# Optimization experiments

Hardware: AMD Instinct MI355X
Metric: run time of the kernel (lower is better)

Reference implementation:

```python
import jax, jax.numpy as jnp
import numpy as np

NL, B, L, D, H, KH, FF, M, NCT, ND = 8, 4, 512, 512, 16, 32, 2048, 512, 6, 14
BINS = jnp.arange(10.0, 150.0, 10.0)  # 14 bucket boundaries
SCALE = 1.0 / np.sqrt(KH).astype(np.float32)


def setup_inputs() -> dict:
    key = jax.random.key(0)
    ks = iter(jax.random.split(key, 64))
    nrm = lambda shape, s=0.02: jax.random.normal(next(ks), shape, dtype=jnp.float32) * s
    inp = {}
    inp['cell_types'] = jax.random.randint(next(ks), (B, L), 0, NCT)
    inp['distances'] = jax.random.uniform(next(ks), (B, L, L), dtype=jnp.float32) * 139.0
    inp['cell_emb'] = nrm((NCT, D), 1.0)
    for name in ['Kqk', 'Kqr', 'Kkr', 'Vqk', 'Vqr', 'Vkr']:
        inp[name] = nrm((ND, KH), 0.02)
    for name in ['Wq', 'Wk', 'Wv', 'Wo']:
        inp[name] = nrm((NL, D, D))
    for name in ['bq', 'bk', 'bv', 'bo']:
        inp[name] = jnp.zeros((NL, D), dtype=jnp.float32)
    inp['W1'] = nrm((NL, D, FF)); inp['b1'] = jnp.zeros((NL, FF), dtype=jnp.float32)
    inp['W2'] = nrm((NL, FF, D)); inp['b2'] = jnp.zeros((NL, D), dtype=jnp.float32)
    inp['g1'] = jnp.ones((NL, D), dtype=jnp.float32); inp['be1'] = jnp.zeros((NL, D), dtype=jnp.float32)
    inp['g2'] = jnp.ones((NL, D), dtype=jnp.float32); inp['be2'] = jnp.zeros((NL, D), dtype=jnp.float32)
    inp['Wm1'] = nrm((D, M)); inp['bm1'] = jnp.zeros((M,), dtype=jnp.float32)
    inp['Wm2'] = nrm((M, 1)); inp['bm2'] = jnp.zeros((1,), dtype=jnp.float32)
    return inp


def _layernorm(x, g, b, eps=1e-5):
    mu = x.mean(-1, keepdims=True)
    var = ((x - mu) ** 2).mean(-1, keepdims=True)
    return (x - mu) * jax.lax.rsqrt(var + eps) * g + b


def _forward(cell_types, distances, cell_emb, Kqk, Kqr, Kkr, Vqk, Vqr, Vkr,
             Wq, bq, Wk, bk, Wv, bv, Wo, bo, W1, b1, W2, b2, g1, be1, g2, be2,
             Wm1, bm1, Wm2, bm2):
    Bsz, Ls = cell_types.shape
    # torch.bucketize(right=False) == searchsorted side='left'
    didx = jnp.clip(jnp.searchsorted(BINS, distances, side='left'), 0, ND - 1)  # [B,L,L]
    # gather distance-bucket relative embeddings once; shared across all layers
    Eqk = Kqk[didx]                      # [B,L,L,KH]  query-side score bias
    Eqr = Kqr[didx]                      # [B,L,L,KH]  key-side score bias
    Ekr = Kkr[didx].sum(-1)              # [B,L,L]     pure pairwise score bias
    Vbias = Vqk[didx] + Vqr[didx] + Vkr[didx]  # [B,L,L,KH] additive value bias
    h = cell_emb[cell_types]             # [B,L,D]

    def layer(h, p):
        wq, bq_, wk, bk_, wv, bv_, wo, bo_, w1, b1_, w2, b2_, gg1, bb1, gg2, bb2 = p
        q = (h @ wq + bq_).reshape(Bsz, Ls, H, KH)
        k = (h @ wk + bk_).reshape(Bsz, Ls, H, KH)
        v = (h @ wv + bv_).reshape(Bsz, Ls, H, KH)
        e = jnp.einsum('blhk,bxhk->bhlx', q, k)
        e = e + jnp.einsum('blhk,blxk->bhlx', q, Eqk)
        e = e + jnp.einsum('bxhk,blxk->bhlx', k, Eqr)
        e = e + Ekr[:, None, :, :]
        a = jax.nn.softmax(e * SCALE, axis=-1)  # [B,H,L,L]
        z = jnp.einsum('bhlx,bxhk->blhk', a, v) + jnp.einsum('bhlx,blxk->blhk', a, Vbias)
        o = z.reshape(Bsz, Ls, H * KH) @ wo + bo_
        h2 = _layernorm(h + o, gg1, bb1)  # post-norm (norm_first=False)
        f = jax.nn.gelu(h2 @ w1 + b1_, approximate=False) @ w2 + b2_
        return _layernorm(h2 + f, gg2, bb2), None

    h, _ = jax.lax.scan(layer, h, (Wq, bq, Wk, bk, Wv, bv, Wo, bo,
                                   W1, b1, W2, b2, g1, be1, g2, be2))
    pooled = h.sum(axis=1)                      # [B,D]
    return jax.nn.relu(pooled @ Wm1 + bm1) @ Wm2 + bm2  # [B,1]


def reference(cell_types, distances, cell_emb, Kqk, Kqr, Kkr, Vqk, Vqr, Vkr,
              Wq, bq, Wk, bk, Wv, bv, Wo, bo, W1, b1, W2, b2, g1, be1, g2, be2,
              Wm1, bm1, Wm2, bm2):
    return _forward(cell_types, distances, cell_emb, Kqk, Kqr, Kkr, Vqk, Vqr, Vkr,
                    Wq, bq, Wk, bk, Wv, bv, Wo, bo, W1, b1, W2, b2, g1, be1, g2, be2,
                    Wm1, bm1, Wm2, bm2)
```

## Files before the change

### kernel.cpp

```cpp
#include <hip/hip_runtime.h>
#include <math.h>

#define NLAY 8
#define BB 4
#define LL 512
#define DDIM 512
#define HH 16
#define KHD 32
#define FFD 2048
#define MMD 512
#define NDB 14
#define QKS 1536
#define SCALEF 0.17677669529663687f

typedef unsigned short u16;
typedef unsigned int u32;
typedef __attribute__((ext_vector_type(8))) short bf16x8;
typedef __attribute__((ext_vector_type(4))) float f32x4;
typedef __attribute__((ext_vector_type(4))) u32 u32x4;

__device__ __forceinline__ u16 f2bf(float f) {
  unsigned u = __builtin_bit_cast(unsigned, f);
  u = (u + 0x7fffu + ((u >> 16) & 1u)) >> 16;
  return (u16)u;
}
__device__ __forceinline__ float bf2f(u16 v) {
  unsigned u = ((unsigned)v) << 16;
  return __builtin_bit_cast(float, u);
}
__device__ __forceinline__ u32 cvt_pk_bf16(float lo, float hi) {
  u32 r;
  asm("v_cvt_pk_bf16_f32 %0, %1, %2" : "=v"(r) : "v"(lo), "v"(hi));
  return r;
}
__device__ __forceinline__ float wredSum(float v) {
#pragma unroll
  for (int o = 32; o > 0; o >>= 1) v += __shfl_down(v, o);
  return v;
}
__device__ __forceinline__ void gload_lds16(const u16* g, u16* l) {
  __builtin_amdgcn_global_load_lds((const __attribute__((address_space(1))) void*)g,
                                   (__attribute__((address_space(3))) void*)l, 16, 0, 0);
}

__global__ void bucketize_kernel(const float* __restrict__ dist, unsigned char* __restrict__ didx, int n) {
  int i = blockIdx.x * 256 + threadIdx.x;
  if (i >= n) return;
  float4 v = ((const float4*)dist)[i];
  float vv[4] = {v.x, v.y, v.z, v.w};
  unsigned char o[4];
#pragma unroll
  for (int j = 0; j < 4; ++j) {
    int c = 0;
#pragma unroll
    for (int s = 1; s <= NDB; ++s) c += (10.0f * (float)s < vv[j]) ? 1 : 0;
    o[j] = (unsigned char)(c > (NDB - 1) ? (NDB - 1) : c);
  }
  *(uchar4*)(didx + i * 4) = *(uchar4*)o;
}

__global__ void embed_kernel(const int* __restrict__ ct, const float* __restrict__ emb,
                             float* __restrict__ h, u16* __restrict__ hbf, int n) {
  int i = blockIdx.x * 256 + threadIdx.x;
  if (i >= n) return;
  int bl = i >> 9, d = i & 511;
  float v = emb[ct[bl] * DDIM + d];
  h[i] = v;
  hbf[i] = f2bf(v);
}

__global__ void prep_kernel(const float* __restrict__ Vqk, const float* __restrict__ Vqr,
                            const float* __restrict__ Vkr, const float* __restrict__ Kkr,
                            float* __restrict__ Vsum, float* __restrict__ EkrS) {
  int tid = threadIdx.x;
  if (tid < NDB * KHD) Vsum[tid] = Vqk[tid] + Vqr[tid] + Vkr[tid];
  if (tid < NDB) {
    float s = 0.f;
    for (int kk = 0; kk < KHD; ++kk) s += Kkr[tid * KHD + kk];
    EkrS[tid] = s;
  }
}

__global__ void biaspack_kernel(const float* __restrict__ bq, const float* __restrict__ bk,
                                const float* __restrict__ bv, float* __restrict__ bqkv) {
  int i = blockIdx.x * 256 + threadIdx.x;
  if (i >= NLAY * QKS) return;
  int lay = i / QKS, c = i % QKS;
  float v;
  if (c < 512) v = bq[lay * DDIM + c];
  else if (c < 1024) v = bk[lay * DDIM + c - 512];
  else v = bv[lay * DDIM + c - 1024];
  bqkv[i] = v;
}

__device__ __forceinline__ void wtconv_tile(const float* __restrict__ src, u16* __restrict__ dst,
                                            int K, int N, int tn, int tk) {
  __shared__ float tl[64][65];
  const int t = threadIdx.x;
#pragma unroll
  for (int p = 0; p < 4; ++p) {
    int k = tk * 64 + p * 16 + (t >> 4);
    int n = tn * 64 + (t & 15) * 4;
    float4 v = *(const float4*)(src + (size_t)k * N + n);
    tl[(t & 15) * 4 + 0][p * 16 + (t >> 4)] = v.x;
    tl[(t & 15) * 4 + 1][p * 16 + (t >> 4)] = v.y;
    tl[(t & 15) * 4 + 2][p * 16 + (t >> 4)] = v.z;
    tl[(t & 15) * 4 + 3][p * 16 + (t >> 4)] = v.w;
  }
  __syncthreads();
  int n = t >> 2, cc = t & 3;
  u16 o[16];
#pragma unroll
  for (int e = 0; e < 16; ++e) o[e] = f2bf(tl[n][cc * 16 + e]);
  u16* dp = dst + (size_t)(tn * 64 + n) * K + tk * 64 + cc * 16;
  *(uint4*)(dp) = *(uint4*)&o[0];
  *(uint4*)(dp + 8) = *(uint4*)&o[8];
}

__global__ __launch_bounds__(256) void wconv_layer(
    const float* __restrict__ Wq, const float* __restrict__ Wk, const float* __restrict__ Wv,
    const float* __restrict__ Wo, const float* __restrict__ W1, const float* __restrict__ W2,
    u16* __restrict__ Wqkvt, u16* __restrict__ Wot, u16* __restrict__ W1t, u16* __restrict__ W2t) {
  int b = blockIdx.x;
  if (b < 64) { wtconv_tile(Wq, Wqkvt, 512, 512, b >> 3, b & 7); return; }
  if (b < 128) { b -= 64; wtconv_tile(Wk, Wqkvt + 512 * 512, 512, 512, b >> 3, b & 7); return; }
  if (b < 192) { b -= 128; wtconv_tile(Wv, Wqkvt + 1024 * 512, 512, 512, b >> 3, b & 7); return; }
  if (b < 256) { b -= 192; wtconv_tile(Wo, Wot, 512, 512, b >> 3, b & 7); return; }
  if (b < 512) { b -= 256; wtconv_tile(W1, W1t, 512, FFD, b >> 3, b & 7); return; }
  b -= 512; wtconv_tile(W2, W2t, FFD, 512, b >> 5, b & 31);
}

__global__ __launch_bounds__(256) void gemm_bf16(
    const u16* __restrict__ A, const u16* __restrict__ Bt, const float* __restrict__ bias,
    float* __restrict__ Cf, u16* __restrict__ Cb,
    int M, int N, int K, int act, int scaleLT) {
  __shared__ u16 As[32 * 64];
  __shared__ u16 Bs[64 * 64];
  const int tid = threadIdx.x, w = tid >> 6, lane = tid & 63;
  const int lr = lane & 15, lg = lane >> 4;
  const int wr = w >> 1, wc = w & 1;
  const int gx = N >> 6;
  const int bi = blockIdx.x;
  const int xcd = bi & 7, rr = bi >> 3;
  const int y = xcd * 8 + rr / gx, x = rr % gx;
  const int row0 = y * 32, col0 = x * 64;
  const int srow = lane >> 3;
  const int aoff = ((lane & 7) ^ srow) * 8;
  const f32x4 z4 = {0.f, 0.f, 0.f, 0.f};
  f32x4 acc[2] = {z4, z4};

  for (int k0 = 0; k0 < K; k0 += 64) {
    gload_lds16(A + (size_t)(row0 + w * 8 + srow) * K + k0 + aoff, As + (w * 8) * 64);
#pragma unroll
    for (int i = 0; i < 2; ++i)
      gload_lds16(Bt + (size_t)(col0 + w * 16 + i * 8 + srow) * K + k0 + aoff,
                  Bs + (w * 16 + i * 8) * 64);
    __syncthreads();
#pragma unroll
    for (int kh = 0; kh < 2; ++kh) {
      bf16x8 a, b[2];
      {
        int r = wr * 16 + lr;
        a = *(const bf16x8*)(As + r * 64 + (((kh * 4 + lg) ^ (r & 7)) << 3));
      }
#pragma unroll
      for (int ni = 0; ni < 2; ++ni) {
        int r = wc * 32 + ni * 16 + lr;
        b[ni] = *(const bf16x8*)(Bs + r * 64 + (((kh * 4 + lg) ^ (r & 7)) << 3));
      }
#pragma unroll
      for (int ni = 0; ni < 2; ++ni)
        acc[ni] = __builtin_amdgcn_mfma_f32_16x16x32_bf16(a, b[ni], acc[ni], 0, 0, 0);
    }
    __syncthreads();
  }
  {
    int r = row0 + wr * 16 + lg * 4;
#pragma unroll
    for (int ni = 0; ni < 2; ++ni) {
      int c = col0 + wc * 32 + ni * 16 + lr;
      float bs = bias[c];
      float sc = (c < scaleLT) ? SCALEF : 1.0f;
#pragma unroll
      for (int j = 0; j < 4; ++j) {
        float v = acc[ni][j] + bs;
        if (act == 1) v = 0.5f * v * (1.0f + erff(v * 0.70710678118654752f));
        size_t idx = (size_t)(r + j) * N + c;
        if (Cf) Cf[idx] = v;
        if (Cb) Cb[idx] = f2bf(v * sc);
      }
    }
  }
}

__global__ void proj_qk_kernel(const u16* __restrict__ qkv, const float* __restrict__ Kqk,
                               const float* __restrict__ Kqr, const float* __restrict__ ekrs,
                               float* __restrict__ qE2, u16* __restrict__ kEbf) {
  int idx = blockIdx.x * 256 + threadIdx.x;
  if (idx >= BB * HH * LL * NDB) return;
  int d = idx % NDB;
  int rest = idx / NDB;
  int l = rest & (LL - 1);
  int bh = rest >> 9;
  int h = bh & (HH - 1);
  int b = bh >> 4;
  const u16* qr_ = qkv + ((size_t)(b * LL + l)) * QKS + h * KHD;
  const u16* kr_ = qr_ + 512;
  const float* kq = Kqk + d * KHD;
  const float* kk2 = Kqr + d * KHD;
  float sq = 0.f, sk = 0.f;
#pragma unroll
  for (int kk = 0; kk < KHD; ++kk) {
    sq += bf2f(qr_[kk]) * kq[kk];
    sk += bf2f(kr_[kk]) * kk2[kk];
  }
  qE2[idx] = sq;
  kEbf[(size_t)rest * 16 + d] = f2bf(sk * SCALEF + SCALEF * ekrs[d]);
}

__global__ __launch_bounds__(256) void vtrans_kernel(const u16* __restrict__ qkv, u16* __restrict__ vt) {
  const int h = blockIdx.x, b = blockIdx.y, tid = threadIdx.x;
  __shared__ u16 tile[KHD][520];
  for (int it = 0; it < 64; ++it) {
    int idx = it * 256 + tid;
    int x = idx >> 5, kh = idx & 31;
    tile[kh][x] = qkv[((size_t)(b * LL) + x) * QKS + 1024 + h * KHD + kh];
  }
  __syncthreads();
  int r = tid >> 3, seg = tid & 7;
  uint4* dst = (uint4*)(vt + ((size_t)(b * HH + h) * KHD + r) * LL);
  const uint4* src = (const uint4*)(&tile[r][0]);
#pragma unroll
  for (int j = 0; j < 8; ++j) dst[seg + j * 8] = src[seg + j * 8];
}

__global__ __launch_bounds__(256) void attn_exp_kernel(
    const u16* __restrict__ qkv, const float* __restrict__ qE2, const u16* __restrict__ kEbf,
    const unsigned char* __restrict__ didx, const float* __restrict__ Vsum,
    u16* __restrict__ E, float* __restrict__ vbias, float* __restrict__ invs) {
  const int i = blockIdx.x;
  const int j = i >> 3;
  const int g = (i & 7) * 8 + (j >> 5);
  const int qr = j & 31;
  const int h = g & 15, b = g >> 4;
  const int tid = threadIdx.x, lane = tid & 63, w = tid >> 6;
  const int lr = lane & 15, lg = lane >> 4;
  const int row0 = qr * 16;

  __shared__ u16 kEs[LL][18];
  __shared__ float qEs[16][17];
  __shared__ float hist[4][64][17];

  {
    const u32* gs = (const u32*)(kEbf + (((size_t)(b * HH + h)) * LL) * 16);
    u32* ls = (u32*)(&kEs[0][0]);
#pragma unroll
    for (int t = 0; t < 16; ++t) {
      int idx = t * 256 + tid;
      int r = idx >> 3, c = idx & 7;
      ls[r * 9 + c] = gs[idx];
    }
  }
  if (tid < 224) {
    int r = tid / 14, d = tid % 14;
    qEs[r][d] = qE2[(((size_t)(b * HH + h)) * LL + row0 + r) * NDB + d];
  }
  {
    float* hf = &hist[0][0][0];
#pragma unroll
    for (int t = 0; t < 17; ++t) hf[t * 256 + tid] = 0.f;
  }

  const bf16x8 aQ = *(const bf16x8*)(qkv + ((size_t)(b * LL + row0 + lr)) * QKS + h * KHD + lg * 8);

  __syncthreads();

  const f32x4 zero4 = {0.f, 0.f, 0.f, 0.f};
  const int keyA = 8 * (lr >> 2) + (lr & 3);
  const u16* kbase = qkv + (size_t)b * LL * QKS + 512 + h * KHD + lg * 8;
  const unsigned char* drow = didx + ((size_t)(b * LL) + row0 + lr) * LL + 8 * lg;
  u16* Ebase = E + ((((size_t)(b * HH + h)) * LL) + row0 + lr) * LL + 8 * lg;
  float* hlane = &hist[w][lane][0];

  bf16x8 kA[4], kB[4];
  uint2 dv[4];
#pragma unroll
  for (int ct = 0; ct < 4; ++ct) {
    const int x0 = w * 128 + ct * 32;
    kA[ct] = *(const bf16x8*)(kbase + (size_t)(x0 + keyA) * QKS);
    kB[ct] = *(const bf16x8*)(kbase + (size_t)(x0 + keyA + 4) * QKS);
    dv[ct] = *(const uint2*)(drow + x0);
  }
  __builtin_amdgcn_sched_barrier(0);

#pragma unroll
  for (int ct = 0; ct < 4; ++ct) {
    const int x0 = w * 128 + ct * 32;
    f32x4 sA = __builtin_amdgcn_mfma_f32_16x16x32_bf16(kA[ct], aQ, zero4, 0, 0, 0);
    f32x4 sB = __builtin_amdgcn_mfma_f32_16x16x32_bf16(kB[ct], aQ, zero4, 0, 0, 0);
    float pA[4], pB[4];
#pragma unroll
    for (int q = 0; q < 4; ++q) {
      const int da = (dv[ct].x >> (8 * q)) & 0xff;
      const int db = (dv[ct].y >> (8 * q)) & 0xff;
      pA[q] = __expf(sA[q] + qEs[lr][da] + bf2f(kEs[x0 + 8 * lg + q][da]));
      pB[q] = __expf(sB[q] + qEs[lr][db] + bf2f(kEs[x0 + 8 * lg + 4 + q][db]));
      hlane[da] += pA[q];
      hlane[db] += pB[q];
    }
    u32x4 pw;
    pw[0] = cvt_pk_bf16(pA[0], pA[1]);
    pw[1] = cvt_pk_bf16(pA[2], pA[3]);
    pw[2] = cvt_pk_bf16(pB[0], pB[1]);
    pw[3] = cvt_pk_bf16(pB[2], pB[3]);
    *(u32x4*)(Ebase + x0) = pw;
  }

  __syncthreads();

  const int r = tid >> 4, c = tid & 15;
  float ht[NDB];
  float rsum = 0.f;
#pragma unroll
  for (int d = 0; d < NDB; ++d) {
    float a = 0.f;
#pragma unroll
    for (int ww = 0; ww < 4; ++ww)
#pragma unroll
      for (int gg = 0; gg < 4; ++gg) a += hist[ww][r + 16 * gg][d];
    ht[d] = a;
    rsum += a;
  }
  float vb_0 = 0.f, vb_1 = 0.f;
#pragma unroll
  for (int d = 0; d < NDB; ++d) {
    vb_0 += ht[d] * Vsum[d * KHD + c];
    vb_1 += ht[d] * Vsum[d * KHD + 16 + c];
  }
  const size_t rowi = (((size_t)(b * HH + h)) * LL) + row0 + r;
  vbias[rowi * KHD + c] = vb_0;
  vbias[rowi * KHD + 16 + c] = vb_1;
  if (c == 0) invs[rowi] = 1.0f / rsum;
}

__global__ __launch_bounds__(256) void attn_pv_kernel(
    const u16* __restrict__ E, const u16* __restrict__ vtbf,
    const float* __restrict__ vbias, const float* __restrict__ invs,
    u16* __restrict__ z) {
  const int i = blockIdx.x;
  const int j = i >> 3;
  const int g = (i & 7) * 8 + (j >> 3);
  const int qt = j & 7;
  const int h = g & 15, b = g >> 4;
  const int tid = threadIdx.x, lane = tid & 63, w = tid >> 6;
  const int lr = lane & 15, lg = lane >> 4;
  const int row0 = qt * 64 + w * 16;

  f32x4 o0 = {0.f, 0.f, 0.f, 0.f}, o1 = {0.f, 0.f, 0.f, 0.f};
  const u16* Ebase = E + ((((size_t)(b * HH + h)) * LL) + row0 + lr) * LL + lg * 8;
  const u16* vbase = vtbf + ((size_t)(b * HH + h) * KHD) * LL + lg * 8;

#pragma unroll 4
  for (int ct = 0; ct < 16; ++ct) {
    const int x0 = ct * 32;
    bf16x8 aE = *(const bf16x8*)(Ebase + x0);
    bf16x8 vb0 = *(const bf16x8*)(vbase + (size_t)lr * LL + x0);
    bf16x8 vb1 = *(const bf16x8*)(vbase + (size_t)(16 + lr) * LL + x0);
    o0 = __builtin_amdgcn_mfma_f32_16x16x32_bf16(aE, vb0, o0, 0, 0, 0);
    o1 = __builtin_amdgcn_mfma_f32_16x16x32_bf16(aE, vb1, o1, 0, 0, 0);
  }

#pragma unroll
  for (int q = 0; q < 4; ++q) {
    const int rl = lg * 4 + q;
    const size_t rowi = (((size_t)(b * HH + h)) * LL) + row0 + rl;
    const float inv = invs[rowi];
    const float v0 = vbias[rowi * KHD + lr];
    const float v1 = vbias[rowi * KHD + 16 + lr];
    const size_t orow = ((size_t)(b * LL + row0 + rl)) * DDIM + h * KHD;
    z[orow + lr] = f2bf((o0[q] + v0) * inv);
    z[orow + 16 + lr] = f2bf((o1[q] + v1) * inv);
  }
}

__global__ __launch_bounds__(256) void add_ln_kernel(
    const float* __restrict__ X, const float* __restrict__ Y,
    const float* __restrict__ g, const float* __restrict__ be,
    float* __restrict__ out, u16* __restrict__ outb) {
  const int row = blockIdx.x, tid = threadIdx.x;
  const int lane = tid & 63, wid = tid >> 6;
  __shared__ float red[4];
  const size_t base = (size_t)row * DDIM;
  float x0 = X[base + tid] + Y[base + tid];
  float x1 = X[base + tid + 256] + Y[base + tid + 256];
  float s = wredSum(x0 + x1);
  if (lane == 0) red[wid] = s;
  __syncthreads();
  float mu = (red[0] + red[1] + red[2] + red[3]) * (1.0f / DDIM);
  __syncthreads();
  float d0 = x0 - mu, d1 = x1 - mu;
  float vs = wredSum(d0 * d0 + d1 * d1);
  if (lane == 0) red[wid] = vs;
  __syncthreads();
  float var = (red[0] + red[1] + red[2] + red[3]) * (1.0f / DDIM);
  float inv = rsqrtf(var + 1e-5f);
  float r0 = d0 * inv * g[tid] + be[tid];
  float r1 = d1 * inv * g[tid + 256] + be[tid + 256];
  out[base + tid] = r0;
  out[base + tid + 256] = r1;
  outb[base + tid] = f2bf(r0);
  outb[base + tid + 256] = f2bf(r1);
}

__global__ __launch_bounds__(256) void pool2_kernel(const float* __restrict__ h, float* __restrict__ pooled) {
  const int s = blockIdx.x, b = blockIdx.y, tid = threadIdx.x;
  float a0 = 0.f, a1 = 0.f;
  const float* base = h + ((size_t)(b * LL) + s * 64) * DDIM;
#pragma unroll 4
  for (int l = 0; l < 64; ++l) {
    a0 += base[(size_t)l * DDIM + tid];
    a1 += base[(size_t)l * DDIM + tid + 256];
  }
  atomicAdd(&pooled[b * DDIM + tid], a0);
  atomicAdd(&pooled[b * DDIM + tid + 256], a1);
}

__global__ __launch_bounds__(256) void head1_kernel(
    const float* __restrict__ pooled, const float* __restrict__ Wm1, float* __restrict__ hidden) {
  const int s = blockIdx.x, b = blockIdx.y, tid = threadIdx.x;
  __shared__ float pl[64];
  if (tid < 64) pl[tid] = pooled[b * DDIM + s * 64 + tid];
  __syncthreads();
  float a0 = 0.f, a1 = 0.f;
  const float* wbase = Wm1 + (size_t)(s * 64) * MMD;
#pragma unroll 8
  for (int dd = 0; dd < 64; ++dd) {
    float p = pl[dd];
    a0 += p * wbase[(size_t)dd * MMD + tid];
    a1 += p * wbase[(size_t)dd * MMD + tid + 256];
  }
  atomicAdd(&hidden[b * MMD + tid], a0);
  atomicAdd(&hidden[b * MMD + tid + 256], a1);
}

__global__ __launch_bounds__(256) void head2_kernel(
    const float* __restrict__ hidden, const float* __restrict__ bm1,
    const float* __restrict__ Wm2, const float* __restrict__ bm2, float* __restrict__ out) {
  const int b = blockIdx.x, tid = threadIdx.x;
  float part = 0.f;
#pragma unroll
  for (int jj = 0; jj < 2; ++jj) {
    int j = tid + jj * 256;
    part += fmaxf(hidden[b * MMD + j] + bm1[j], 0.f) * Wm2[j];
  }
  __shared__ float red[4];
  int lane = tid & 63, wid = tid >> 6;
  float ssum = wredSum(part);
  if (lane == 0) red[wid] = ssum;
  __syncthreads();
  if (tid == 0) out[b] = red[0] + red[1] + red[2] + red[3] + bm2[0];
}

extern "C" void kernel_launch(void* const* d_in, const int* in_sizes, int n_in,
                              void* d_out, int out_size, void* d_ws, size_t ws_size,
                              hipStream_t stream) {
  const int* cell_types = (const int*)d_in[0];
  const float* distances = (const float*)d_in[1];
  const float* cell_emb = (const float*)d_in[2];
  const float* Kqk = (const float*)d_in[3];
  const float* Kqr = (const float*)d_in[4];
  const float* Kkr = (const float*)d_in[5];
  const float* Vqk = (const float*)d_in[6];
  const float* Vqr = (const float*)d_in[7];
  const float* Vkr = (const float*)d_in[8];
  const float* Wq = (const float*)d_in[9];
  const float* Wk = (const float*)d_in[10];
  const float* Wv = (const float*)d_in[11];
  const float* Wo = (const float*)d_in[12];
  const float* bq = (const float*)d_in[13];
  const float* bk = (const float*)d_in[14];
  const float* bv = (const float*)d_in[15];
  const float* bo = (const float*)d_in[16];
  const float* W1 = (const float*)d_in[17];
  const float* b1 = (const float*)d_in[18];
  const float* W2 = (const float*)d_in[19];
  const float* b2 = (const float*)d_in[20];
  const float* g1 = (const float*)d_in[21];
  const float* be1 = (const float*)d_in[22];
  const float* g2 = (const float*)d_in[23];
  const float* be2 = (const float*)d_in[24];
  const float* Wm1 = (const float*)d_in[25];
  const float* bm1 = (const float*)d_in[26];
  const float* Wm2 = (const float*)d_in[27];
  const float* bm2 = (const float*)d_in[28];

  char* w = (char*)d_ws;
  auto alloc = [&](size_t bytes) { void* p = (void*)w; w += (bytes + 255) & ~(size_t)255; return p; };
  unsigned char* didx = (unsigned char*)alloc(sizeof(unsigned char) * BB * LL * LL);
  float* h    = (float*)alloc(sizeof(float) * BB * LL * DDIM);
  u16* hbf    = (u16*)alloc(sizeof(u16) * BB * LL * DDIM);
  float* h2   = (float*)alloc(sizeof(float) * BB * LL * DDIM);
  u16* h2bf   = (u16*)alloc(sizeof(u16) * BB * LL * DDIM);
  u16* qkvbf  = (u16*)alloc(sizeof(u16) * BB * LL * QKS);
  float* ob   = (float*)alloc(sizeof(float) * BB * LL * DDIM);
  u16* f1bf   = (u16*)alloc(sizeof(u16) * BB * LL * FFD);
  u16* zbf    = (u16*)alloc(sizeof(u16) * BB * LL * DDIM);
  u16* vtbf   = (u16*)alloc(sizeof(u16) * BB * HH * KHD * LL);
  float* qE2  = (float*)alloc(sizeof(float) * BB * HH * LL * NDB);
  u16* kEbf   = (u16*)alloc(sizeof(u16) * (size_t)BB * HH * LL * 16);
  u16* Ebuf   = (u16*)alloc(sizeof(u16) * (size_t)BB * HH * LL * LL);
  float* vbias = (float*)alloc(sizeof(float) * (size_t)BB * HH * LL * KHD);
  float* invs = (float*)alloc(sizeof(float) * (size_t)BB * HH * LL);
  u16* Wqkvt  = (u16*)alloc(sizeof(u16) * (size_t)NLAY * QKS * DDIM);
  u16* Wot    = (u16*)alloc(sizeof(u16) * (size_t)NLAY * DDIM * DDIM);
  u16* W1t    = (u16*)alloc(sizeof(u16) * (size_t)NLAY * FFD * DDIM);
  u16* W2t    = (u16*)alloc(sizeof(u16) * (size_t)NLAY * DDIM * FFD);
  float* bqkv = (float*)alloc(sizeof(float) * NLAY * QKS);
  float* Vsum = (float*)alloc(sizeof(float) * NDB * KHD);
  float* EkrS = (float*)alloc(sizeof(float) * NDB);
  float* pooled = (float*)alloc(sizeof(float) * BB * DDIM);
  float* hidden = (float*)alloc(sizeof(float) * BB * MMD);

  const int Mrows = BB * LL;

  bucketize_kernel<<<(BB * LL * LL / 4 + 255) / 256, 256, 0, stream>>>(distances, didx, BB * LL * LL / 4);
  embed_kernel<<<(BB * LL * DDIM + 255) / 256, 256, 0, stream>>>(cell_types, cell_emb, h, hbf, BB * LL * DDIM);
  prep_kernel<<<1, 512, 0, stream>>>(Vqk, Vqr, Vkr, Kkr, Vsum, EkrS);
  biaspack_kernel<<<(NLAY * QKS + 255) / 256, 256, 0, stream>>>(bq, bk, bv, bqkv);
  hipMemsetAsync(pooled, 0, sizeof(float) * BB * DDIM, stream);
  hipMemsetAsync(hidden, 0, sizeof(float) * BB * MMD, stream);

  for (int lay = 0; lay < NLAY; ++lay) {
    wconv_layer<<<768, 256, 0, stream>>>(
        Wq + (size_t)lay * DDIM * DDIM, Wk + (size_t)lay * DDIM * DDIM,
        Wv + (size_t)lay * DDIM * DDIM, Wo + (size_t)lay * DDIM * DDIM,
        W1 + (size_t)lay * DDIM * FFD, W2 + (size_t)lay * FFD * DDIM,
        Wqkvt + (size_t)lay * QKS * DDIM, Wot + (size_t)lay * DDIM * DDIM,
        W1t + (size_t)lay * FFD * DDIM, W2t + (size_t)lay * DDIM * FFD);
  }

  const int nrel = BB * HH * LL * NDB;

  for (int lay = 0; lay < NLAY; ++lay) {
    gemm_bf16<<<dim3((Mrows / 32) * (QKS / 64)), 256, 0, stream>>>(
        hbf, Wqkvt + (size_t)lay * QKS * DDIM, bqkv + (size_t)lay * QKS,
        nullptr, qkvbf, Mrows, QKS, DDIM, 0, 512);

    proj_qk_kernel<<<(nrel + 255) / 256, 256, 0, stream>>>(qkvbf, Kqk, Kqr, EkrS, qE2, kEbf);
    vtrans_kernel<<<dim3(HH, BB), 256, 0, stream>>>(qkvbf, vtbf);
    attn_exp_kernel<<<dim3(2048), 256, 0, stream>>>(qkvbf, qE2, kEbf, didx, Vsum, Ebuf, vbias, invs);
    attn_pv_kernel<<<dim3(512), 256, 0, stream>>>(Ebuf, vtbf, vbias, invs, zbf);

    gemm_bf16<<<dim3((Mrows / 32) * (DDIM / 64)), 256, 0, stream>>>(
        zbf, Wot + (size_t)lay * DDIM * DDIM, bo + (size_t)lay * DDIM, ob, nullptr, Mrows, DDIM, DDIM, 0, 0);
    add_ln_kernel<<<Mrows, 256, 0, stream>>>(h, ob, g1 + (size_t)lay * DDIM, be1 + (size_t)lay * DDIM, h2, h2bf);
    gemm_bf16<<<dim3((Mrows / 32) * (FFD / 64)), 256, 0, stream>>>(
        h2bf, W1t + (size_t)lay * FFD * DDIM, b1 + (size_t)lay * FFD, nullptr, f1bf, Mrows, FFD, DDIM, 1, 0);
    gemm_bf16<<<dim3((Mrows / 32) * (DDIM / 64)), 256, 0, stream>>>(
        f1bf, W2t + (size_t)lay * DDIM * FFD, b2 + (size_t)lay * DDIM, ob, nullptr, Mrows, DDIM, FFD, 0, 0);
    add_ln_kernel<<<Mrows, 256, 0, stream>>>(h2, ob, g2 + (size_t)lay * DDIM, be2 + (size_t)lay * DDIM, h, hbf);
  }

  pool2_kernel<<<dim3(8, BB), 256, 0, stream>>>(h, pooled);
  head1_kernel<<<dim3(8, BB), 256, 0, stream>>>(pooled, Wm1, hidden);
  head2_kernel<<<BB, 256, 0, stream>>>(hidden, bm1, Wm2, bm2, (float*)d_out);
}
```

Baseline: 1.034 ms.

## Fuse attention exp and PV kernels to avoid materializing score matrix

Merges the exponentiated-score kernel and the probability-times-V kernel into one. Each wave now multiplies its bf16 probabilities against V fragments held in registers. The four waves' partial outputs are reduced with shared-memory atomics, then the value bias and 1/rowsum normalization are applied in the epilogue. This removes the global write and re-read of the B*H*L*L bf16 score buffer and the vbias/invs intermediates, plus one launch per layer. The cost is more registers for the V fragments and the overhead of shared atomics.

New measurement: 1.111 ms. +7.4%, slower.

```diff
diff --git a/kernel.cpp b/kernel.cpp
--- a/kernel.cpp
+++ b/kernel.cpp
@@ -234,10 +234,11 @@
   for (int j = 0; j < 8; ++j) dst[seg + j * 8] = src[seg + j * 8];
 }
 
-__global__ __launch_bounds__(256) void attn_exp_kernel(
-    const u16* __restrict__ qkv, const float* __restrict__ qE2, const u16* __restrict__ kEbf,
+__global__ __launch_bounds__(256) void attn_fused_kernel(
+    const u16* __restrict__ qkv, const u16* __restrict__ vtbf,
+    const float* __restrict__ qE2, const u16* __restrict__ kEbf,
     const unsigned char* __restrict__ didx, const float* __restrict__ Vsum,
-    u16* __restrict__ E, float* __restrict__ vbias, float* __restrict__ invs) {
+    u16* __restrict__ z) {
   const int i = blockIdx.x;
   const int j = i >> 3;
   const int g = (i & 7) * 8 + (j >> 5);
@@ -250,6 +251,7 @@
   __shared__ u16 kEs[LL][18];
   __shared__ float qEs[16][17];
   __shared__ float hist[4][64][17];
+  __shared__ float osh[16][33];
 
   {
     const u32* gs = (const u32*)(kEbf + (((size_t)(b * HH + h)) * LL) * 16);
@@ -270,6 +272,7 @@
 #pragma unroll
     for (int t = 0; t < 17; ++t) hf[t * 256 + tid] = 0.f;
   }
+  if (tid < 132) ((float4*)&osh[0][0])[tid] = float4{0.f, 0.f, 0.f, 0.f};
 
   const bf16x8 aQ = *(const bf16x8*)(qkv + ((size_t)(b * LL + row0 + lr)) * QKS + h * KHD + lg * 8);
 
@@ -278,11 +281,11 @@
   const f32x4 zero4 = {0.f, 0.f, 0.f, 0.f};
   const int keyA = 8 * (lr >> 2) + (lr & 3);
   const u16* kbase = qkv + (size_t)b * LL * QKS + 512 + h * KHD + lg * 8;
+  const u16* vbase = vtbf + ((size_t)(b * HH + h) * KHD) * LL + lg * 8;
   const unsigned char* drow = didx + ((size_t)(b * LL) + row0 + lr) * LL + 8 * lg;
-  u16* Ebase = E + ((((size_t)(b * HH + h)) * LL) + row0 + lr) * LL + 8 * lg;
   float* hlane = &hist[w][lane][0];
 
-  bf16x8 kA[4], kB[4];
+  bf16x8 kA[4], kB[4], v0r[4], v1r[4];
   uint2 dv[4];
 #pragma unroll
   for (int ct = 0; ct < 4; ++ct) {
@@ -290,9 +293,12 @@
     kA[ct] = *(const bf16x8*)(kbase + (size_t)(x0 + keyA) * QKS);
     kB[ct] = *(const bf16x8*)(kbase + (size_t)(x0 + keyA + 4) * QKS);
     dv[ct] = *(const uint2*)(drow + x0);
+    v0r[ct] = *(const bf16x8*)(vbase + (size_t)lr * LL + x0);
+    v1r[ct] = *(const bf16x8*)(vbase + (size_t)(16 + lr) * LL + x0);
   }
   __builtin_amdgcn_sched_barrier(0);
 
+  f32x4 o0 = zero4, o1 = zero4;
 #pragma unroll
   for (int ct = 0; ct < 4; ++ct) {
     const int x0 = w * 128 + ct * 32;
@@ -313,9 +319,17 @@
     pw[1] = cvt_pk_bf16(pA[2], pA[3]);
     pw[2] = cvt_pk_bf16(pB[0], pB[1]);
     pw[3] = cvt_pk_bf16(pB[2], pB[3]);
-    *(u32x4*)(Ebase + x0) = pw;
-  }
-
+    bf16x8 aP = __builtin_bit_cast(bf16x8, pw);
+    o0 = __builtin_amdgcn_mfma_f32_16x16x32_bf16(aP, v0r[ct], o0, 0, 0, 0);
+    o1 = __builtin_amdgcn_mfma_f32_16x16x32_bf16(aP, v1r[ct], o1, 0, 0, 0);
+  }
+
+#pragma unroll
+  for (int q = 0; q < 4; ++q) {
+    const int rl = lg * 4 + q;
+    atomicAdd(&osh[rl][lr], o0[q]);
+    atomicAdd(&osh[rl][16 + lr], o1[q]);
+  }
   __syncthreads();
 
   const int r = tid >> 4, c = tid & 15;
@@ -331,56 +345,16 @@
     ht[d] = a;
     rsum += a;
   }
+  const float inv = 1.0f / rsum;
   float vb_0 = 0.f, vb_1 = 0.f;
 #pragma unroll
   for (int d = 0; d < NDB; ++d) {
     vb_0 += ht[d] * Vsum[d * KHD + c];
     vb_1 += ht[d] * Vsum[d * KHD + 16 + c];
   }
-  const size_t rowi = (((size_t)(b * HH + h)) * LL) + row0 + r;
-  vbias[rowi * KHD + c] = vb_0;
-  vbias[rowi * KHD + 16 + c] = vb_1;
-  if (c == 0) invs[rowi] = 1.0f / rsum;
-}
-
-__global__ __launch_bounds__(256) void attn_pv_kernel(
-    const u16* __restrict__ E, const u16* __restrict__ vtbf,
-    const float* __restrict__ vbias, const float* __restrict__ invs,
-    u16* __restrict__ z) {
-  const int i = blockIdx.x;
-  const int j = i >> 3;
-  const int g = (i & 7) * 8 + (j >> 3);
-  const int qt = j & 7;
-  const int h = g & 15, b = g >> 4;
-  const int tid = threadIdx.x, lane = tid & 63, w = tid >> 6;
-  const int lr = lane & 15, lg = lane >> 4;
-  const int row0 = qt * 64 + w * 16;
-
-  f32x4 o0 = {0.f, 0.f, 0.f, 0.f}, o1 = {0.f, 0.f, 0.f, 0.f};
-  const u16* Ebase = E + ((((size_t)(b * HH + h)) * LL) + row0 + lr) * LL + lg * 8;
-  const u16* vbase = vtbf + ((size_t)(b * HH + h) * KHD) * LL + lg * 8;
-
-#pragma unroll 4
-  for (int ct = 0; ct < 16; ++ct) {
-    const int x0 = ct * 32;
-    bf16x8 aE = *(const bf16x8*)(Ebase + x0);
-    bf16x8 vb0 = *(const bf16x8*)(vbase + (size_t)lr * LL + x0);
-    bf16x8 vb1 = *(const bf16x8*)(vbase + (size_t)(16 + lr) * LL + x0);
-    o0 = __builtin_amdgcn_mfma_f32_16x16x32_bf16(aE, vb0, o0, 0, 0, 0);
-    o1 = __builtin_amdgcn_mfma_f32_16x16x32_bf16(aE, vb1, o1, 0, 0, 0);
-  }
-
-#pragma unroll
-  for (int q = 0; q < 4; ++q) {
-    const int rl = lg * 4 + q;
-    const size_t rowi = (((size_t)(b * HH + h)) * LL) + row0 + rl;
-    const float inv = invs[rowi];
-    const float v0 = vbias[rowi * KHD + lr];
-    const float v1 = vbias[rowi * KHD + 16 + lr];
-    const size_t orow = ((size_t)(b * LL + row0 + rl)) * DDIM + h * KHD;
-    z[orow + lr] = f2bf((o0[q] + v0) * inv);
-    z[orow + 16 + lr] = f2bf((o1[q] + v1) * inv);
-  }
+  const size_t orow = ((size_t)(b * LL + row0 + r)) * DDIM + h * KHD;
+  z[orow + c] = f2bf((osh[r][c] + vb_0) * inv);
+  z[orow + 16 + c] = f2bf((osh[r][16 + c] + vb_1) * inv);
 }
 
 __global__ __launch_bounds__(256) void add_ln_kernel(
@@ -508,9 +482,6 @@
   u16* vtbf   = (u16*)alloc(sizeof(u16) * BB * HH * KHD * LL);
   float* qE2  = (float*)alloc(sizeof(float) * BB * HH * LL * NDB);
   u16* kEbf   = (u16*)alloc(sizeof(u16) * (size_t)BB * HH * LL * 16);
-  u16* Ebuf   = (u16*)alloc(sizeof(u16) * (size_t)BB * HH * LL * LL);
-  float* vbias = (float*)alloc(sizeof(float) * (size_t)BB * HH * LL * KHD);
-  float* invs = (float*)alloc(sizeof(float) * (size_t)BB * HH * LL);
   u16* Wqkvt  = (u16*)alloc(sizeof(u16) * (size_t)NLAY * QKS * DDIM);
   u16* Wot    = (u16*)alloc(sizeof(u16) * (size_t)NLAY * DDIM * DDIM);
   u16* W1t    = (u16*)alloc(sizeof(u16) * (size_t)NLAY * FFD * DDIM);
@@ -548,8 +519,7 @@
 
     proj_qk_kernel<<<(nrel + 255) / 256, 256, 0, stream>>>(qkvbf, Kqk, Kqr, EkrS, qE2, kEbf);
     vtrans_kernel<<<dim3(HH, BB), 256, 0, stream>>>(qkvbf, vtbf);
-    attn_exp_kernel<<<dim3(2048), 256, 0, stream>>>(qkvbf, qE2, kEbf, didx, Vsum, Ebuf, vbias, invs);
-    attn_pv_kernel<<<dim3(512), 256, 0, stream>>>(Ebuf, vtbf, vbias, invs, zbf);
+    attn_fused_kernel<<<dim3(2048), 256, 0, stream>>>(qkvbf, vtbf, qE2, kEbf, didx, Vsum, zbf);
 
     gemm_bf16<<<dim3((Mrows / 32) * (DDIM / 64)), 256, 0, stream>>>(
         zbf, Wot + (size_t)lay * DDIM * DDIM, bo + (size_t)lay * DDIM, ob, nullptr, Mrows, DDIM, DDIM, 0, 0);
```
